# Optimization experiments

Measured on AMD Instinct MI355X. Metric: run time of the kernel, lower is better.

## Reference

```python
import jax, jax.numpy as jnp
import numpy as np
from jax import lax

N, CIN, COUT, H, W = 16, 512, 256, 32, 32
EPS = 1e-5


def _conv(x, w, b, pad_h, pad_w):
    # x: [N,Cin,H,W], w: [Cout,Cin,kh,kw], pad = ((top,bottom),(left,right))
    y = lax.conv_general_dilated(
        x, w, window_strides=(1, 1), padding=(pad_h, pad_w),
        dimension_numbers=("NCHW", "OIHW", "NCHW"))
    return y + b[None, :, None, None]


def setup_inputs() -> dict:
    key = jax.random.key(0)
    ks = jax.random.split(key, 12)
    s = 0.02
    return {
        "x": jax.random.normal(ks[0], (N, CIN, H, W), jnp.float32),
        "w1": jax.random.normal(ks[1], (COUT, CIN, 3, 3), jnp.float32) * s,
        "b1": jax.random.normal(ks[2], (COUT,), jnp.float32) * s,
        "w2": jax.random.normal(ks[3], (COUT, CIN, 2, 3), jnp.float32) * s,
        "b2": jax.random.normal(ks[4], (COUT,), jnp.float32) * s,
        "w3": jax.random.normal(ks[5], (COUT, CIN, 3, 2), jnp.float32) * s,
        "b3": jax.random.normal(ks[6], (COUT,), jnp.float32) * s,
        "w4": jax.random.normal(ks[7], (COUT, CIN, 2, 2), jnp.float32) * s,
        "b4": jax.random.normal(ks[8], (COUT,), jnp.float32) * s,
        "gamma": jnp.ones((COUT,), jnp.float32),
        "beta": jnp.zeros((COUT,), jnp.float32),
    }


def reference(x, w1, b1, w2, b2, w3, b3, w4, b4, gamma, beta):
    # torch F.pad(l,r,t,b) -> lax padding ((top,bottom),(left,right))
    o1 = _conv(x, w1, b1, (1, 1), (1, 1))  # 3x3, pad (1,1,1,1) -> [N,Cout,H,W]
    o2 = _conv(x, w2, b2, (1, 0), (1, 1))  # 2x3, pad (1,1,1,0)
    o3 = _conv(x, w3, b3, (1, 1), (1, 0))  # 3x2, pad (1,0,1,1)
    o4 = _conv(x, w4, b4, (1, 0), (1, 0))  # 2x2, pad (1,0,1,0)
    # pixel-shuffle interleave: o1->(even,even), o2->(odd,even), o3->(even,odd), o4->(odd,odd)
    row_even = jnp.stack([o1, o3], axis=-1).reshape(N, COUT, H, 2 * W)
    row_odd = jnp.stack([o2, o4], axis=-1).reshape(N, COUT, H, 2 * W)
    y = jnp.stack([row_even, row_odd], axis=-2).reshape(N, COUT, 2 * H, 2 * W)
    # BatchNorm2d, training mode: biased batch stats over (N,H,W)
    mean = jnp.mean(y, axis=(0, 2, 3), keepdims=True)
    var = jnp.mean(jnp.square(y - mean), axis=(0, 2, 3), keepdims=True)
    normed = (y - mean) * lax.rsqrt(var + EPS)
    normed = normed * gamma[None, :, None, None] + beta[None, :, None, None]
    return jax.nn.relu(normed)
```

## Files before the change

### kernel.cpp

```cpp
#include <hip/hip_runtime.h>
#include <hip/hip_bf16.h>


typedef unsigned short ushort_t;
typedef __attribute__((ext_vector_type(8))) short short8;
typedef __attribute__((ext_vector_type(4))) float floatx4;
typedef __attribute__((ext_vector_type(2))) float floatx2;
typedef __attribute__((ext_vector_type(4))) unsigned short u16x4;
typedef __attribute__((ext_vector_type(8))) unsigned short u16x8;
typedef __attribute__((ext_vector_type(4))) unsigned int u32x4;

#define XT_OFF    0u
#define WT_OFF    18939904u
#define BIAS_OFF  28377088u
#define STATS_OFF 28381184u

#define NSITES 204

#define ASYNC16(g, l) __builtin_amdgcn_global_load_lds( \
    (const __attribute__((address_space(1))) void*)(g), \
    (__attribute__((address_space(3))) void*)(l), 16, 0, 0)

__device__ __forceinline__ ushort_t f2bf(float f) {
  unsigned int u = __builtin_bit_cast(unsigned int, f);
  u += 0x7fffu + ((u >> 16) & 1u);
  return (ushort_t)(u >> 16);
}

__global__ __launch_bounds__(256) void prep_x(const float* __restrict__ x,
                                              ushort_t* __restrict__ xt) {
  const int b = blockIdx.x;
  const int n = b / 34, hp = b % 34;
  const int t = threadIdx.x;
  ushort_t* dst = xt + (size_t)(n * 34 + hp) * (34 * 512);
  if (hp == 0 || hp == 33) {
    u32x4 z = {0u, 0u, 0u, 0u};
    for (int i = t; i < 2176; i += 256) ((u32x4*)dst)[i] = z;
    return;
  }
  const int h = hp - 1;
  {
    u32x4 z = {0u, 0u, 0u, 0u};
    if (t < 64) ((u32x4*)dst)[t] = z;
    else if (t < 128) ((u32x4*)(dst + 33 * 512))[t - 64] = z;
  }
  __shared__ ushort_t lds[128 * 36];
  const size_t base = (size_t)n * 524288 + (size_t)h * 32;
  for (int ci0 = 0; ci0 < 512; ci0 += 128) {
    __syncthreads();
    {
      const int cil = t >> 3;
      const int w4 = (t & 7) << 2;
#pragma unroll
      for (int cc = 0; cc < 4; ++cc) {
        const int ci = cil + cc * 32;
        floatx4 v = *(const floatx4*)(x + base + (size_t)(ci0 + ci) * 1024 + w4);
        u16x4 hv;
#pragma unroll
        for (int j = 0; j < 4; ++j) hv[j] = f2bf(v[j]);
        *(u16x4*)&lds[ci * 36 + w4] = hv;
      }
    }
    __syncthreads();
    {
      const int w = t & 31;
      const int j8 = t >> 5;
#pragma unroll
      for (int cc2 = 0; cc2 < 2; ++cc2) {
        const int cil = cc2 * 64 + j8 * 8;
        u16x8 v;
#pragma unroll
        for (int j = 0; j < 8; ++j) v[j] = lds[(cil + j) * 36 + w];
        *(u16x8*)(dst + (w + 1) * 512 + ci0 + cil) = v;
      }
    }
  }
}

__global__ __launch_bounds__(256) void prep_w(
    const float* __restrict__ w1, const float* __restrict__ w2,
    const float* __restrict__ w3, const float* __restrict__ w4,
    const float* __restrict__ b1, const float* __restrict__ b2,
    const float* __restrict__ b3, const float* __restrict__ b4,
    ushort_t* __restrict__ wt, float* __restrict__ bias) {
  const int nout = blockIdx.x;
  const int q = nout >> 8, co = nout & 255;
  const int row = co * 4 + q;
  const int t = threadIdx.x;
  const float* wsrc; const float* bsrc; int khl, kwl;
  if (q == 0)      { wsrc = w1; bsrc = b1; khl = 3; kwl = 3; }
  else if (q == 1) { wsrc = w2; bsrc = b2; khl = 2; kwl = 3; }
  else if (q == 2) { wsrc = w3; bsrc = b3; khl = 3; kwl = 2; }
  else             { wsrc = w4; bsrc = b4; khl = 2; kwl = 2; }
  if (t == 0) bias[row] = bsrc[co];
  ushort_t* dst = wt + (size_t)row * 4608;
  for (int tap = 0; tap < 9; ++tap) {
    const int dh = tap / 3, dw = tap % 3;
    const bool valid = (dh < khl) && (dw < kwl);
#pragma unroll
    for (int cc = 0; cc < 2; ++cc) {
      const int ci = cc * 256 + t;
      ushort_t v = 0;
      if (valid) v = f2bf(wsrc[(((size_t)co * 512 + ci) * khl + dh) * kwl + dw]);
      dst[tap * 512 + ci] = v;
    }
  }
}

__global__ void zero_stats(float* __restrict__ stats) {
  stats[threadIdx.x] = 0.f;
}

__global__ __launch_bounds__(256) void gemm_kernel(
    const ushort_t* __restrict__ xt, const ushort_t* __restrict__ wt,
    const float* __restrict__ bias, float* __restrict__ out,
    float* __restrict__ stats) {
  __shared__ char ldsX[NSITES * 128];
  __shared__ char ldsW[2][128 * 128];
  const int tid = threadIdx.x;
  const int bx = blockIdx.x;
  const int bn = bx & 7, bm = bx >> 3;
  const int n0 = bn << 7;
  const int n_img = bm >> 3;
  const int h0p = (bm & 7) << 2;
  const int wv = tid >> 6, lane = tid & 63;
  const int ri = lane & 15, kg = lane >> 4;
  const int wm = (wv & 1) << 6, wn = (wv >> 1) << 6;

  const char* xgp[7];
  char* xlp[7];
  {
    const char* xg = (const char*)(xt + (size_t)(n_img * 34 + h0p) * (34 * 512));
#pragma unroll
    for (int p = 0; p < 7; ++p) {
      const int idx = p * 256 + tid;
      const int site = idx >> 3, slot = idx & 7;
      const int c = slot ^ (site & 7);
      xgp[p] = xg + site * 1024 + (c << 4);
      xlp[p] = ldsX + idx * 16;
    }
  }
  const char* wgp[4];
  char* wlp0[4];
  char* wlp1[4];
#pragma unroll
  for (int p = 0; p < 4; ++p) {
    const int idx = p * 256 + tid;
    const int row = idx >> 3, slot = idx & 7;
    const int c = slot ^ (row & 7);
    wgp[p] = (const char*)wt + (size_t)(n0 + row) * 9216 + (c << 4);
    wlp0[p] = ldsW[0] + idx * 16;
    wlp1[p] = ldsW[1] + idx * 16;
  }

  floatx4 acc[4][4] = {};

  int arow[4], bsite[4];
#pragma unroll
  for (int f = 0; f < 4; ++f) arow[f] = wn + (f << 4) + ri;
#pragma unroll
  for (int fj = 0; fj < 4; ++fj)
    bsite[fj] = ((wm >> 5) + (fj >> 1)) * 34 + ((fj & 1) << 4) + ri;

  for (int chunk = 0; chunk < 8; ++chunk) {
    const int cb = chunk << 7;
#pragma unroll
    for (int p = 0; p < 6; ++p) ASYNC16(xgp[p] + cb, xlp[p]);
    if (tid < 96) ASYNC16(xgp[6] + cb, xlp[6]);
#pragma unroll
    for (int p = 0; p < 4; ++p) ASYNC16(wgp[p] + cb, wlp0[p]);
    __syncthreads();
#pragma unroll
    for (int tap = 0; tap < 9; ++tap) {
      if (tap < 8) {
        const int noff = ((tap + 1) << 10) + cb;
        if (tap & 1) {
#pragma unroll
          for (int p = 0; p < 4; ++p) ASYNC16(wgp[p] + noff, wlp0[p]);
        } else {
#pragma unroll
          for (int p = 0; p < 4; ++p) ASYNC16(wgp[p] + noff, wlp1[p]);
        }
      }
      const char* wb = ldsW[tap & 1];
      const int tapo = ((tap / 3) * 34 + (tap % 3)) * 128;
#pragma unroll
      for (int ks = 0; ks < 2; ++ks) {
        const int c = (ks << 2) + kg;
        short8 a4[4], b4[4];
#pragma unroll
        for (int f = 0; f < 4; ++f)
          a4[f] = *(const short8*)(wb + arow[f] * 128 +
                                   ((c ^ (arow[f] & 7)) << 4));
#pragma unroll
        for (int fj = 0; fj < 4; ++fj) {
          const int sadr = bsite[fj] * 128 + tapo;
          const int srow = bsite[fj] + (tap / 3) * 34 + (tap % 3);
          b4[fj] = *(const short8*)(ldsX + sadr + ((c ^ (srow & 7)) << 4));
        }
#pragma unroll
        for (int fi = 0; fi < 4; ++fi)
#pragma unroll
          for (int fj = 0; fj < 4; ++fj)
            acc[fi][fj] = __builtin_amdgcn_mfma_f32_16x16x32_bf16(
                a4[fi], b4[fj], acc[fi][fj], 0, 0, 0);
      }
      __syncthreads();
    }
  }

  const int quad = kg, colL = ri;
#pragma unroll
  for (int fi = 0; fi < 4; ++fi) {
    const int co = ((n0 + wn + (fi << 4)) >> 2) + quad;
    const floatx4 bv = *(const floatx4*)(bias + n0 + wn + (fi << 4) + (quad << 2));
    float s = 0.f, s2 = 0.f;
    float* obase = out + ((size_t)(n_img * 256 + co) << 12);
#pragma unroll
    for (int fj = 0; fj < 4; ++fj) {
      const int mb = wm + (fj << 4) + colL;
      const int hl = mb >> 5, w = mb & 31;
      const int h = h0p + hl;
      float v0 = acc[fi][fj][0] + bv[0];
      float v1 = acc[fi][fj][1] + bv[1];
      float v2 = acc[fi][fj][2] + bv[2];
      float v3 = acc[fi][fj][3] + bv[3];
      s += (v0 + v1) + (v2 + v3);
      s2 += v0 * v0 + v1 * v1 + v2 * v2 + v3 * v3;
      float* p = obase + (h << 7) + (w << 1);
      floatx2 e = {v0, v2};
      floatx2 o = {v1, v3};
      *(floatx2*)p = e;
      *(floatx2*)(p + 64) = o;
    }
#pragma unroll
    for (int off = 1; off < 16; off <<= 1) {
      s += __shfl_xor(s, off);
      s2 += __shfl_xor(s2, off);
    }
    if (colL == 0) {
      atomicAdd(&stats[co], s);
      atomicAdd(&stats[256 + co], s2);
    }
  }
}

__global__ __launch_bounds__(256) void bn_apply(
    float* __restrict__ y, const float* __restrict__ stats,
    const float* __restrict__ gamma, const float* __restrict__ beta) {
  const int b = blockIdx.x;
  const int co = b & 255;
  const int t = threadIdx.x;
  const float mean = stats[co] * (1.f / 65536.f);
  const float var = stats[256 + co] * (1.f / 65536.f) - mean * mean;
  const float rstd = rsqrtf(var + 1e-5f);
  const float scale = rstd * gamma[co];
  const float shift = beta[co] - mean * scale;
  float* p = y + (size_t)b * 4096;
#pragma unroll
  for (int it = 0; it < 4; ++it) {
    floatx4* q = (floatx4*)(p + (it * 256 + t) * 4);
    floatx4 v = *q;
#pragma unroll
    for (int e = 0; e < 4; ++e) v[e] = fmaxf(v[e] * scale + shift, 0.f);
    *q = v;
  }
}

extern "C" void kernel_launch(void* const* d_in, const int* in_sizes, int n_in,
                              void* d_out, int out_size, void* d_ws,
                              size_t ws_size, hipStream_t stream) {
  const float* x  = (const float*)d_in[0];
  const float* w1 = (const float*)d_in[1];
  const float* b1 = (const float*)d_in[2];
  const float* w2 = (const float*)d_in[3];
  const float* b2 = (const float*)d_in[4];
  const float* w3 = (const float*)d_in[5];
  const float* b3 = (const float*)d_in[6];
  const float* w4 = (const float*)d_in[7];
  const float* b4 = (const float*)d_in[8];
  const float* gamma = (const float*)d_in[9];
  const float* beta  = (const float*)d_in[10];
  float* out = (float*)d_out;

  char* ws = (char*)d_ws;
  ushort_t* xt   = (ushort_t*)(ws + XT_OFF);
  ushort_t* wt   = (ushort_t*)(ws + WT_OFF);
  float*    bias = (float*)(ws + BIAS_OFF);
  float*    st   = (float*)(ws + STATS_OFF);

  zero_stats<<<1, 512, 0, stream>>>(st);
  prep_x<<<16 * 34, 256, 0, stream>>>(x, xt);
  prep_w<<<1024, 256, 0, stream>>>(w1, w2, w3, w4, b1, b2, b3, b4, wt, bias);
  gemm_kernel<<<1024, 256, 0, stream>>>(xt, wt, bias, out, st);
  bn_apply<<<4096, 256, 0, stream>>>(out, st, gamma, beta);
}
```

Before: 270.6 us.

## Group weight rows by sub-kernel and skip zero-padded taps in GEMM

Weight rows are reordered so each GEMM N-block holds a single sub-convolution (3x3, 2x3, 3x2, 2x2). The tap loop then walks only that sub-kernel's valid taps through a packed tap list, dropping the MFMA work and weight loads spent on zero-padded taps. The epilogue becomes per-channel scalar strided stores, giving up the paired float2 stores. Separately, the three prep launches (stats zeroing, x transpose, weight pack) are merged into one kernel to cut launch overhead. Because blocks now do 4, 6 or 9 taps, work per block is uneven.

```diff
diff --git a/kernel.cpp b/kernel.cpp
--- a/kernel.cpp
+++ b/kernel.cpp
@@ -5,7 +5,6 @@
 typedef unsigned short ushort_t;
 typedef __attribute__((ext_vector_type(8))) short short8;
 typedef __attribute__((ext_vector_type(4))) float floatx4;
-typedef __attribute__((ext_vector_type(2))) float floatx2;
 typedef __attribute__((ext_vector_type(4))) unsigned short u16x4;
 typedef __attribute__((ext_vector_type(8))) unsigned short u16x8;
 typedef __attribute__((ext_vector_type(4))) unsigned int u32x4;
@@ -27,11 +26,43 @@
   return (ushort_t)(u >> 16);
 }
 
-__global__ __launch_bounds__(256) void prep_x(const float* __restrict__ x,
-                                              ushort_t* __restrict__ xt) {
+__global__ __launch_bounds__(256) void prep_all(
+    const float* __restrict__ x, ushort_t* __restrict__ xt,
+    const float* __restrict__ w1, const float* __restrict__ w2,
+    const float* __restrict__ w3, const float* __restrict__ w4,
+    const float* __restrict__ b1, const float* __restrict__ b2,
+    const float* __restrict__ b3, const float* __restrict__ b4,
+    ushort_t* __restrict__ wt, float* __restrict__ bias,
+    float* __restrict__ stats) {
+  __shared__ ushort_t lds[128 * 36];
+  const int t = threadIdx.x;
+  if (blockIdx.x >= 544) {
+    const int nout = blockIdx.x - 544;
+    if (nout == 0 && t < 256) { stats[t] = 0.f; stats[256 + t] = 0.f; }
+    const int q = nout >> 8, co = nout & 255;
+    const float* wsrc; const float* bsrc; int khl, kwl;
+    if (q == 0)      { wsrc = w1; bsrc = b1; khl = 3; kwl = 3; }
+    else if (q == 1) { wsrc = w2; bsrc = b2; khl = 2; kwl = 3; }
+    else if (q == 2) { wsrc = w3; bsrc = b3; khl = 3; kwl = 2; }
+    else             { wsrc = w4; bsrc = b4; khl = 2; kwl = 2; }
+    if (t == 0) bias[nout] = bsrc[co];
+    ushort_t* dst = wt + (size_t)nout * 4608;
+    for (int tap = 0; tap < 9; ++tap) {
+      const int dh = tap / 3, dw = tap % 3;
+      const bool valid = (dh < khl) && (dw < kwl);
+#pragma unroll
+      for (int cc = 0; cc < 2; ++cc) {
+        const int ci = cc * 256 + t;
+        ushort_t v = 0;
+        if (valid)
+          v = f2bf(wsrc[(((size_t)co * 512 + ci) * khl + dh) * kwl + dw]);
+        dst[tap * 512 + ci] = v;
+      }
+    }
+    return;
+  }
   const int b = blockIdx.x;
   const int n = b / 34, hp = b % 34;
-  const int t = threadIdx.x;
   ushort_t* dst = xt + (size_t)(n * 34 + hp) * (34 * 512);
   if (hp == 0 || hp == 33) {
     u32x4 z = {0u, 0u, 0u, 0u};
@@ -44,7 +75,6 @@
     if (t < 64) ((u32x4*)dst)[t] = z;
     else if (t < 128) ((u32x4*)(dst + 33 * 512))[t - 64] = z;
   }
-  __shared__ ushort_t lds[128 * 36];
   const size_t base = (size_t)n * 524288 + (size_t)h * 32;
   for (int ci0 = 0; ci0 < 512; ci0 += 128) {
     __syncthreads();
@@ -75,40 +105,6 @@
       }
     }
   }
-}
-
-__global__ __launch_bounds__(256) void prep_w(
-    const float* __restrict__ w1, const float* __restrict__ w2,
-    const float* __restrict__ w3, const float* __restrict__ w4,
-    const float* __restrict__ b1, const float* __restrict__ b2,
-    const float* __restrict__ b3, const float* __restrict__ b4,
-    ushort_t* __restrict__ wt, float* __restrict__ bias) {
-  const int nout = blockIdx.x;
-  const int q = nout >> 8, co = nout & 255;
-  const int row = co * 4 + q;
-  const int t = threadIdx.x;
-  const float* wsrc; const float* bsrc; int khl, kwl;
-  if (q == 0)      { wsrc = w1; bsrc = b1; khl = 3; kwl = 3; }
-  else if (q == 1) { wsrc = w2; bsrc = b2; khl = 2; kwl = 3; }
-  else if (q == 2) { wsrc = w3; bsrc = b3; khl = 3; kwl = 2; }
-  else             { wsrc = w4; bsrc = b4; khl = 2; kwl = 2; }
-  if (t == 0) bias[row] = bsrc[co];
-  ushort_t* dst = wt + (size_t)row * 4608;
-  for (int tap = 0; tap < 9; ++tap) {
-    const int dh = tap / 3, dw = tap % 3;
-    const bool valid = (dh < khl) && (dw < kwl);
-#pragma unroll
-    for (int cc = 0; cc < 2; ++cc) {
-      const int ci = cc * 256 + t;
-      ushort_t v = 0;
-      if (valid) v = f2bf(wsrc[(((size_t)co * 512 + ci) * khl + dh) * kwl + dw]);
-      dst[tap * 512 + ci] = v;
-    }
-  }
-}
-
-__global__ void zero_stats(float* __restrict__ stats) {
-  stats[threadIdx.x] = 0.f;
 }
 
 __global__ __launch_bounds__(256) void gemm_kernel(
@@ -121,11 +117,17 @@
   const int bx = blockIdx.x;
   const int bn = bx & 7, bm = bx >> 3;
   const int n0 = bn << 7;
+  const int q = bn >> 1;
   const int n_img = bm >> 3;
   const int h0p = (bm & 7) << 2;
   const int wv = tid >> 6, lane = tid & 63;
   const int ri = lane & 15, kg = lane >> 4;
   const int wm = (wv & 1) << 6, wn = (wv >> 1) << 6;
+
+  const unsigned long long pack =
+      (q == 0) ? 0x876543210ull : (q == 1) ? 0x543210ull
+                                : (q == 2) ? 0x764310ull : 0x4310ull;
+  const int T = (q == 0) ? 9 : (q == 3) ? 4 : 6;
 
   const char* xgp[7];
   char* xlp[7];
@@ -154,7 +156,6 @@
   }
 
   floatx4 acc[4][4] = {};
-
   int arow[4], bsite[4];
 #pragma unroll
   for (int f = 0; f < 4; ++f) arow[f] = wn + (f << 4) + ri;
@@ -162,19 +163,21 @@
   for (int fj = 0; fj < 4; ++fj)
     bsite[fj] = ((wm >> 5) + (fj >> 1)) * 34 + ((fj & 1) << 4) + ri;
 
+  const int tap0off = ((int)(pack & 15)) << 10;
   for (int chunk = 0; chunk < 8; ++chunk) {
     const int cb = chunk << 7;
 #pragma unroll
     for (int p = 0; p < 6; ++p) ASYNC16(xgp[p] + cb, xlp[p]);
     if (tid < 96) ASYNC16(xgp[6] + cb, xlp[6]);
 #pragma unroll
-    for (int p = 0; p < 4; ++p) ASYNC16(wgp[p] + cb, wlp0[p]);
+    for (int p = 0; p < 4; ++p) ASYNC16(wgp[p] + tap0off + cb, wlp0[p]);
     __syncthreads();
-#pragma unroll
-    for (int tap = 0; tap < 9; ++tap) {
-      if (tap < 8) {
-        const int noff = ((tap + 1) << 10) + cb;
-        if (tap & 1) {
+    for (int i = 0; i < T; ++i) {
+      const int tap = (int)((pack >> (4 * i)) & 15);
+      if (i < T - 1) {
+        const int ntap = (int)((pack >> (4 * i + 4)) & 15);
+        const int noff = (ntap << 10) + cb;
+        if (i & 1) {
 #pragma unroll
           for (int p = 0; p < 4; ++p) ASYNC16(wgp[p] + noff, wlp0[p]);
         } else {
@@ -182,8 +185,9 @@
           for (int p = 0; p < 4; ++p) ASYNC16(wgp[p] + noff, wlp1[p]);
         }
       }
-      const char* wb = ldsW[tap & 1];
-      const int tapo = ((tap / 3) * 34 + (tap % 3)) * 128;
+      const char* wb = ldsW[i & 1];
+      const int tapsite = tap + 31 * ((tap * 11) >> 5);
+      const int tapo = tapsite * 128;
 #pragma unroll
       for (int ks = 0; ks < 2; ++ks) {
         const int c = (ks << 2) + kg;
@@ -194,9 +198,9 @@
                                    ((c ^ (arow[f] & 7)) << 4));
 #pragma unroll
         for (int fj = 0; fj < 4; ++fj) {
-          const int sadr = bsite[fj] * 128 + tapo;
-          const int srow = bsite[fj] + (tap / 3) * 34 + (tap % 3);
-          b4[fj] = *(const short8*)(ldsX + sadr + ((c ^ (srow & 7)) << 4));
+          const int srow = bsite[fj] + tapsite;
+          b4[fj] = *(const short8*)(ldsX + bsite[fj] * 128 + tapo +
+                                    ((c ^ (srow & 7)) << 4));
         }
 #pragma unroll
         for (int fi = 0; fi < 4; ++fi)
@@ -210,37 +214,33 @@
   }
 
   const int quad = kg, colL = ri;
+  const int ph = q & 1, pw = q >> 1;
 #pragma unroll
   for (int fi = 0; fi < 4; ++fi) {
-    const int co = ((n0 + wn + (fi << 4)) >> 2) + quad;
-    const floatx4 bv = *(const floatx4*)(bias + n0 + wn + (fi << 4) + (quad << 2));
-    float s = 0.f, s2 = 0.f;
-    float* obase = out + ((size_t)(n_img * 256 + co) << 12);
-#pragma unroll
-    for (int fj = 0; fj < 4; ++fj) {
-      const int mb = wm + (fj << 4) + colL;
-      const int hl = mb >> 5, w = mb & 31;
-      const int h = h0p + hl;
-      float v0 = acc[fi][fj][0] + bv[0];
-      float v1 = acc[fi][fj][1] + bv[1];
-      float v2 = acc[fi][fj][2] + bv[2];
-      float v3 = acc[fi][fj][3] + bv[3];
-      s += (v0 + v1) + (v2 + v3);
-      s2 += v0 * v0 + v1 * v1 + v2 * v2 + v3 * v3;
-      float* p = obase + (h << 7) + (w << 1);
-      floatx2 e = {v0, v2};
-      floatx2 o = {v1, v3};
-      *(floatx2*)p = e;
-      *(floatx2*)(p + 64) = o;
-    }
-#pragma unroll
-    for (int off = 1; off < 16; off <<= 1) {
-      s += __shfl_xor(s, off);
-      s2 += __shfl_xor(s2, off);
-    }
-    if (colL == 0) {
-      atomicAdd(&stats[co], s);
-      atomicAdd(&stats[256 + co], s2);
+#pragma unroll
+    for (int reg = 0; reg < 4; ++reg) {
+      const int co = ((bn & 1) << 7) + wn + (fi << 4) + (quad << 2) + reg;
+      const float bv = bias[(q << 8) + co];
+      float s = 0.f, s2 = 0.f;
+      float* obase = out + ((size_t)(n_img * 256 + co) << 12) + (ph << 6) + pw;
+#pragma unroll
+      for (int fj = 0; fj < 4; ++fj) {
+        const int mb = wm + (fj << 4) + colL;
+        const int h = h0p + (mb >> 5), w = mb & 31;
+        const float v = acc[fi][fj][reg] + bv;
+        s += v;
+        s2 += v * v;
+        obase[(h << 7) + (w << 1)] = v;
+      }
+#pragma unroll
+      for (int off = 1; off < 16; off <<= 1) {
+        s += __shfl_xor(s, off);
+        s2 += __shfl_xor(s2, off);
+      }
+      if (colL == 0) {
+        atomicAdd(&stats[co], s);
+        atomicAdd(&stats[256 + co], s2);
+      }
     }
   }
 }
@@ -259,11 +259,11 @@
   float* p = y + (size_t)b * 4096;
 #pragma unroll
   for (int it = 0; it < 4; ++it) {
-    floatx4* q = (floatx4*)(p + (it * 256 + t) * 4);
-    floatx4 v = *q;
+    floatx4* qp = (floatx4*)(p + (it * 256 + t) * 4);
+    floatx4 v = *qp;
 #pragma unroll
     for (int e = 0; e < 4; ++e) v[e] = fmaxf(v[e] * scale + shift, 0.f);
-    *q = v;
+    *qp = v;
   }
 }
 
@@ -289,9 +289,8 @@
   float*    bias = (float*)(ws + BIAS_OFF);
   float*    st   = (float*)(ws + STATS_OFF);
 
-  zero_stats<<<1, 512, 0, stream>>>(st);
-  prep_x<<<16 * 34, 256, 0, stream>>>(x, xt);
-  prep_w<<<1024, 256, 0, stream>>>(w1, w2, w3, w4, b1, b2, b3, b4, wt, bias);
+  prep_all<<<544 + 1024, 256, 0, stream>>>(x, xt, w1, w2, w3, w4,
+                                           b1, b2, b3, b4, wt, bias, st);
   gemm_kernel<<<1024, 256, 0, stream>>>(xt, wt, bias, out, st);
   bn_apply<<<4096, 256, 0, stream>>>(out, st, gamma, beta);
 }
```

Result: slower. 336.7 us (+24.4%).
